# Performance work log

Measured on AMD Instinct MI355X. Metric: run time of the kernel, lower is better.

Reference implementation:

```python
import jax, jax.numpy as jnp
import numpy as np


def gcn_conv(x, W, b, src, dst, n_nodes):
    """PyG GCNConv: linear transform, add self-loops, symmetric deg^-1/2 norm, scatter-add, bias."""
    h = x @ W  # [N, out] transform first (out_dim <= in_dim keeps gather traffic low)
    loop = jnp.arange(n_nodes)
    s = jnp.concatenate([src, loop])  # sources incl. self-loops
    d = jnp.concatenate([dst, loop])  # targets incl. self-loops
    deg = jnp.zeros((n_nodes,), h.dtype).at[d].add(jnp.ones((), h.dtype))
    dinv = jax.lax.rsqrt(deg)  # deg >= 1 because of self-loops
    coef = (dinv[s] * dinv[d])[:, None]  # [E+N, 1]
    out = jax.ops.segment_sum(h[s] * coef, d, num_segments=n_nodes)
    return out + b


def setup_inputs() -> dict:
    key = jax.random.key(0)
    k1, k2, k3, k4 = jax.random.split(key, 4)
    N, E = 100000, 1600000
    IN, HID, OUT = 128, 64, 32
    x = jax.random.normal(k1, (N, IN), dtype=jnp.float32)
    edge_index = jax.random.randint(k2, (2, E), 0, N, dtype=jnp.int64)
    W1 = jax.random.normal(k3, (IN, HID), dtype=jnp.float32) * (1.0 / np.sqrt(IN))
    b1 = jnp.zeros((HID,), jnp.float32)
    W2 = jax.random.normal(k4, (HID, OUT), dtype=jnp.float32) * (1.0 / np.sqrt(HID))
    b2 = jnp.zeros((OUT,), jnp.float32)
    return {"x": x, "edge_index": edge_index, "W1": W1, "b1": b1, "W2": W2, "b2": b2}


def reference(x, edge_index, W1, b1, W2, b2):
    src, dst = edge_index[0], edge_index[1]
    n = x.shape[0]
    h = jax.nn.relu(gcn_conv(x, W1, b1, src, dst, n))
    return gcn_conv(h, W2, b2, src, dst, n)
```

## Files before the change

kernel.cpp:

```cpp
#include <hip/hip_runtime.h>
#include <hip/hip_bf16.h>


#define IN_DIM 128
#define HID_DIM 64
#define OUT_DIM 32
#define BSHIFT 8
#define BSIZE 256
#define BMASK 255
#define PEB 4096
#define CAPSHIFT 13

typedef __attribute__((ext_vector_type(2))) float v2f;

__device__ inline unsigned pack_bf16x2(float a, float b) {
    unsigned ua = __float_as_uint(a), ub = __float_as_uint(b);
    unsigned ra = (ua + 0x7fffu + ((ua >> 16) & 1u)) >> 16;
    unsigned rb = (ub + 0x7fffu + ((ub >> 16) & 1u)) & 0xffff0000u;
    return (ra & 0xffffu) | rb;
}
#define BF_LO(w) __uint_as_float((w) << 16)
#define BF_HI(w) __uint_as_float((w) & 0xffff0000u)

__device__ inline v2f bfpair(unsigned u) {
    v2f r;
    r.x = __uint_as_float(u << 16);
    r.y = __uint_as_float(u & 0xffff0000u);
    return r;
}

#define ACC8(q)                                         \
    do {                                                \
        acc[0] += BF_LO((q).x); acc[1] += BF_HI((q).x); \
        acc[2] += BF_LO((q).y); acc[3] += BF_HI((q).y); \
        acc[4] += BF_LO((q).z); acc[5] += BF_HI((q).z); \
        acc[6] += BF_LO((q).w); acc[7] += BF_HI((q).w); \
    } while (0)

__global__ __launch_bounds__(256) void k_partition(const int* __restrict__ src,
                                                   const int* __restrict__ dst, int E,
                                                   int* __restrict__ bfill,
                                                   unsigned* __restrict__ packed, int B) {
    __shared__ int cnt[512];
    __shared__ int off[512];
    int t = threadIdx.x;
    for (int b = t; b < 512; b += 256) cnt[b] = 0;
    __syncthreads();
    int base = blockIdx.x * PEB;
    int dv[PEB / 256];
#pragma unroll
    for (int i = 0; i < PEB / 256; ++i) {
        int e = base + i * 256 + t;
        dv[i] = (e < E) ? dst[e] : -1;
        if (dv[i] >= 0) atomicAdd(&cnt[dv[i] >> BSHIFT], 1);
    }
    __syncthreads();
    for (int b = t; b < B; b += 256) {
        int c = cnt[b];
        int o = c ? atomicAdd(&bfill[b], c) : 0;
        off[b] = (b << CAPSHIFT) + o;
    }
    __syncthreads();
#pragma unroll
    for (int i = 0; i < PEB / 256; ++i) {
        int e = base + i * 256 + t;
        int d = dv[i];
        if (d >= 0) {
            int s = src[e];
            int slot = atomicAdd(&off[d >> BSHIFT], 1);
            packed[slot] = ((unsigned)s << BSHIFT) | (unsigned)(d & BMASK);
        }
    }
}

__global__ __launch_bounds__(256) void k_csrfill(const unsigned* __restrict__ packed,
                                                 const int* __restrict__ bfill,
                                                 int* __restrict__ colidx,
                                                 uint2* __restrict__ rowptr2,
                                                 float* __restrict__ dinv,
                                                 int N, int B) {
    __shared__ int ldeg[256];
    __shared__ int lscan[256];
    __shared__ int sexc[256];
    __shared__ int lfill[256];
    int t = threadIdx.x, bkt = blockIdx.x;
    int base = bkt << CAPSHIFT;
    int end  = base + bfill[bkt];
    ldeg[t] = 0;
    __syncthreads();
    for (int e = base + t; e < end; e += 256)
        atomicAdd(&ldeg[packed[e] & BMASK], 1);
    __syncthreads();
    int v = ldeg[t];
    lscan[t] = v;
    __syncthreads();
    for (int off = 1; off < 256; off <<= 1) {
        int x = (t >= off) ? lscan[t - off] : 0;
        __syncthreads();
        lscan[t] += x;
        __syncthreads();
    }
    int exc = lscan[t] - v;
    sexc[t] = exc;
    lfill[t] = 0;
    int node = (bkt << BSHIFT) + t;
    if (node < N) {
        rowptr2[node] = make_uint2((unsigned)(base + exc), (unsigned)(base + exc + v));
        dinv[node] = rsqrtf((float)v + 1.0f);
    }
    __syncthreads();
    for (int e = base + t; e < end; e += 256) {
        unsigned w = packed[e];
        int ld = w & BMASK;
        int pos = base + sexc[ld] + atomicAdd(&lfill[ld], 1);
        colidx[pos] = (int)(w >> BSHIFT);
    }
}

__global__ __launch_bounds__(256) void k_gemm1(const float* __restrict__ x,
                                               const float* __restrict__ W,
                                               const float* __restrict__ dinv,
                                               unsigned* __restrict__ g1b, int N) {
    __shared__ float xs[64 * 36];
    __shared__ float ws[32 * 64];
    int t = threadIdx.x;
    int row0 = blockIdx.x * 64;
    int tx = t & 15;
    int ty = t >> 4;
    int sr = t >> 3, sc = t & 7;

    float acc[4][4] = {};
    for (int kt = 0; kt < 4; ++kt) {
        const float4* W4 = (const float4*)(W + kt * 32 * HID_DIM);
        float4* ws4 = (float4*)ws;
        ws4[t] = W4[t];
        ws4[t + 256] = W4[t + 256];
#pragma unroll
        for (int half = 0; half < 2; ++half) {
            int r = sr + half * 32;
            int row = row0 + r;
            float4 val = make_float4(0.f, 0.f, 0.f, 0.f);
            if (row < N)
                val = *(const float4*)&x[(size_t)row * IN_DIM + kt * 32 + sc * 4];
            *(float4*)&xs[r * 36 + sc * 4] = val;
        }
        __syncthreads();
#pragma unroll
        for (int k = 0; k < 32; k += 4) {
            float a[4][4], b[4][4];
#pragma unroll
            for (int i = 0; i < 4; ++i)
                *(float4*)a[i] = *(const float4*)&xs[(ty * 4 + i) * 36 + k];
#pragma unroll
            for (int kk = 0; kk < 4; ++kk)
                *(float4*)b[kk] = *(const float4*)&ws[(k + kk) * HID_DIM + tx * 4];
#pragma unroll
            for (int i = 0; i < 4; ++i)
#pragma unroll
                for (int kk = 0; kk < 4; ++kk)
#pragma unroll
                    for (int j = 0; j < 4; ++j)
                        acc[i][j] += a[i][kk] * b[kk][j];
        }
        __syncthreads();
    }
#pragma unroll
    for (int i = 0; i < 4; ++i) {
        int row = row0 + ty * 4 + i;
        if (row < N) {
            float dv = dinv[row];
            uint2 u;
            u.x = pack_bf16x2(acc[i][0] * dv, acc[i][1] * dv);
            u.y = pack_bf16x2(acc[i][2] * dv, acc[i][3] * dv);
            *(uint2*)&g1b[(size_t)row * 32 + tx * 2] = u;
        }
    }
}

__global__ __launch_bounds__(128) void k_agg1(const unsigned* __restrict__ g1,
                                              const uint2* __restrict__ rowptr2,
                                              const int* __restrict__ colidx,
                                              const float* __restrict__ dinv,
                                              const float* __restrict__ b1,
                                              unsigned* __restrict__ t1b, int N) {
    int t = threadIdx.x;
    int lane = t & 63;
    int q = lane >> 4, ql = lane & 15;
    int grp = ql >> 3, fp = ql & 7;
    int dd = blockIdx.x * 8 + (t >> 6) * 4 + q;
    bool live = dd < N;
    int d = live ? dd : N - 1;

    uint2 be = rowptr2[d];
    v2f a01 = {0.f, 0.f}, a23 = {0.f, 0.f}, a45 = {0.f, 0.f}, a67 = {0.f, 0.f};
#define ACC8V(qv)                                    \
    do {                                             \
        a01 += bfpair((qv).x); a23 += bfpair((qv).y);\
        a45 += bfpair((qv).z); a67 += bfpair((qv).w);\
    } while (0)
    int e = (int)be.x, end = (int)be.y;
    for (; e + 4 <= end; e += 4) {
        int s0 = colidx[e + grp];
        int s1 = colidx[e + 2 + grp];
        uint4 q0 = *(const uint4*)&g1[(size_t)s0 * 32 + fp * 4];
        uint4 q1 = *(const uint4*)&g1[(size_t)s1 * 32 + fp * 4];
        ACC8V(q0);
        ACC8V(q1);
    }
    for (; e + 2 <= end; e += 2) {
        int s = colidx[e + grp];
        uint4 qv = *(const uint4*)&g1[(size_t)s * 32 + fp * 4];
        ACC8V(qv);
    }
    if (e < end) {
        int s = colidx[e];
        uint4 qv = *(const uint4*)&g1[(size_t)s * 32 + fp * 4];
        if (grp == 0) ACC8V(qv);
    }
#undef ACC8V
    float acc[8] = {a01.x, a01.y, a23.x, a23.y, a45.x, a45.y, a67.x, a67.y};
#pragma unroll
    for (int i = 0; i < 8; ++i)
        acc[i] += __shfl_xor(acc[i], 8);

    uint4 sq = *(const uint4*)&g1[(size_t)d * 32 + fp * 4];
    ACC8(sq);
    float dv = dinv[d];
    float4 bb0 = ((const float4*)b1)[fp * 2];
    float4 bb1 = ((const float4*)b1)[fp * 2 + 1];
    float v0 = fmaxf(dv * acc[0] + bb0.x, 0.f);
    float v1 = fmaxf(dv * acc[1] + bb0.y, 0.f);
    float v2 = fmaxf(dv * acc[2] + bb0.z, 0.f);
    float v3 = fmaxf(dv * acc[3] + bb0.w, 0.f);
    float v4 = fmaxf(dv * acc[4] + bb1.x, 0.f);
    float v5 = fmaxf(dv * acc[5] + bb1.y, 0.f);
    float v6 = fmaxf(dv * acc[6] + bb1.z, 0.f);
    float v7 = fmaxf(dv * acc[7] + bb1.w, 0.f);
    if (live && grp == 0) {
        uint4 u;
        u.x = pack_bf16x2(v0, v1);
        u.y = pack_bf16x2(v2, v3);
        u.z = pack_bf16x2(v4, v5);
        u.w = pack_bf16x2(v6, v7);
        *(uint4*)&t1b[(size_t)dd * 32 + fp * 4] = u;
    }
}

__global__ __launch_bounds__(256) void k_gemm2b(const unsigned* __restrict__ t1b,
                                                const float* __restrict__ W2,
                                                const float* __restrict__ dinv,
                                                unsigned* __restrict__ g2b, int N) {
    __shared__ float t1s[64 * 68];
    __shared__ float W2s[HID_DIM * OUT_DIM];
    int t = threadIdx.x;
    int row0 = blockIdx.x * 64;

    const float4* W24 = (const float4*)W2;
    float4* W2s4 = (float4*)W2s;
    W2s4[t] = W24[t];
    W2s4[t + 256] = W24[t + 256];
#pragma unroll
    for (int i = 0; i < 8; ++i) {
        int idx = t + 256 * i;
        int r = idx >> 5, c = idx & 31;
        int grow = row0 + r;
        unsigned u = 0;
        if (grow < N) u = t1b[(size_t)grow * 32 + c];
        float2 f;
        f.x = BF_LO(u);
        f.y = BF_HI(u);
        *(float2*)&t1s[r * 68 + c * 2] = f;
    }
    __syncthreads();

    int ty = t >> 3;
    int tx = t & 7;
    float acc[2][4] = {};
#pragma unroll 4
    for (int k = 0; k < 64; k += 4) {
        float a[2][4], b[4][4];
#pragma unroll
        for (int i = 0; i < 2; ++i)
            *(float4*)a[i] = *(const float4*)&t1s[(ty * 2 + i) * 68 + k];
#pragma unroll
        for (int kk = 0; kk < 4; ++kk)
            *(float4*)b[kk] = *(const float4*)&W2s[(k + kk) * OUT_DIM + tx * 4];
#pragma unroll
        for (int i = 0; i < 2; ++i)
#pragma unroll
            for (int kk = 0; kk < 4; ++kk)
#pragma unroll
                for (int j = 0; j < 4; ++j)
                    acc[i][j] += a[i][kk] * b[kk][j];
    }
#pragma unroll
    for (int i = 0; i < 2; ++i) {
        int row = row0 + ty * 2 + i;
        if (row < N) {
            float dv = dinv[row];
            uint2 u;
            u.x = pack_bf16x2(acc[i][0] * dv, acc[i][1] * dv);
            u.y = pack_bf16x2(acc[i][2] * dv, acc[i][3] * dv);
            *(uint2*)&g2b[(size_t)row * 16 + tx * 2] = u;
        }
    }
}

__global__ __launch_bounds__(128) void k_agg2(const unsigned* __restrict__ g2,
                                              const uint2* __restrict__ rowptr2,
                                              const int* __restrict__ colidx,
                                              const float* __restrict__ dinv,
                                              const float* __restrict__ b2,
                                              float* __restrict__ out, int N) {
    int t = threadIdx.x;
    int lane = t & 63;
    int o = lane >> 3, ol = lane & 7;
    int grp = ol >> 2, fp = ol & 3;
    int dd = blockIdx.x * 16 + (t >> 6) * 8 + o;
    bool live = dd < N;
    int d = live ? dd : N - 1;

    uint2 be = rowptr2[d];
    v2f a01 = {0.f, 0.f}, a23 = {0.f, 0.f}, a45 = {0.f, 0.f}, a67 = {0.f, 0.f};
#define ACC8V(qv)                                    \
    do {                                             \
        a01 += bfpair((qv).x); a23 += bfpair((qv).y);\
        a45 += bfpair((qv).z); a67 += bfpair((qv).w);\
    } while (0)
    int e = (int)be.x, end = (int)be.y;
    for (; e + 4 <= end; e += 4) {
        int s0 = colidx[e + grp];
        int s1 = colidx[e + 2 + grp];
        uint4 q0 = *(const uint4*)&g2[(size_t)s0 * 16 + fp * 4];
        uint4 q1 = *(const uint4*)&g2[(size_t)s1 * 16 + fp * 4];
        ACC8V(q0);
        ACC8V(q1);
    }
    for (; e + 2 <= end; e += 2) {
        int s = colidx[e + grp];
        uint4 qv = *(const uint4*)&g2[(size_t)s * 16 + fp * 4];
        ACC8V(qv);
    }
    if (e < end) {
        int s = colidx[e];
        uint4 qv = *(const uint4*)&g2[(size_t)s * 16 + fp * 4];
        if (grp == 0) ACC8V(qv);
    }
#undef ACC8V
    float acc[8] = {a01.x, a01.y, a23.x, a23.y, a45.x, a45.y, a67.x, a67.y};
#pragma unroll
    for (int i = 0; i < 8; ++i)
        acc[i] += __shfl_xor(acc[i], 4);
    uint4 sq = *(const uint4*)&g2[(size_t)d * 16 + fp * 4];
    ACC8(sq);
    float dv = dinv[d];
    float4 bb0 = ((const float4*)b2)[fp * 2];
    float4 bb1 = ((const float4*)b2)[fp * 2 + 1];
    if (live && grp == 0) {
        float4 r0, r1;
        r0.x = dv * acc[0] + bb0.x; r0.y = dv * acc[1] + bb0.y;
        r0.z = dv * acc[2] + bb0.z; r0.w = dv * acc[3] + bb0.w;
        r1.x = dv * acc[4] + bb1.x; r1.y = dv * acc[5] + bb1.y;
        r1.z = dv * acc[6] + bb1.z; r1.w = dv * acc[7] + bb1.w;
        *(float4*)&out[(size_t)dd * OUT_DIM + fp * 8] = r0;
        *(float4*)&out[(size_t)dd * OUT_DIM + fp * 8 + 4] = r1;
    }
}

extern "C" void kernel_launch(void* const* d_in, const int* in_sizes, int n_in,
                              void* d_out, int out_size, void* d_ws, size_t ws_size,
                              hipStream_t stream) {
    const float* x  = (const float*)d_in[0];
    const int*   ei = (const int*)d_in[1];
    const float* W1 = (const float*)d_in[2];
    const float* b1 = (const float*)d_in[3];
    const float* W2 = (const float*)d_in[4];
    const float* b2 = (const float*)d_in[5];
    float* out = (float*)d_out;

    const int N = in_sizes[0] / IN_DIM;
    const int E = in_sizes[1] / 2;
    const int* src = ei;
    const int* dst = ei + E;

    const int B   = (N + BSIZE - 1) / BSIZE;
    const int nPB = (E + PEB - 1) / PEB;
    const size_t SLOTS = (size_t)B << CAPSHIFT;

    char* p = (char*)d_ws;
    auto alloc = [&](size_t bytes) -> void* {
        void* r = (void*)p;
        p += (bytes + 255) & ~(size_t)255;
        return r;
    };
    int*      bfill   = (int*)alloc((size_t)B * 4);
    unsigned* packed  = (unsigned*)alloc(SLOTS * 4);
    int*      colidx  = (int*)alloc(SLOTS * 4);
    uint2*    rowptr2 = (uint2*)alloc((size_t)N * 8);
    float*    dinv    = (float*)alloc((size_t)N * 4);
    unsigned* g1b     = (unsigned*)alloc((size_t)N * 32 * 4);
    unsigned* t1b     = (unsigned*)alloc((size_t)N * 32 * 4);
    unsigned* g2b     = (unsigned*)alloc((size_t)N * 16 * 4);

    hipMemsetAsync(bfill, 0, (size_t)B * 4, stream);
    k_partition<<<nPB, 256, 0, stream>>>(src, dst, E, bfill, packed, B);
    k_csrfill<<<B, 256, 0, stream>>>(packed, bfill, colidx, rowptr2, dinv, N, B);

    k_gemm1<<<(N + 63) / 64, 256, 0, stream>>>(x, W1, dinv, g1b, N);
    k_agg1<<<(N + 7) / 8, 128, 0, stream>>>(g1b, rowptr2, colidx, dinv, b1, t1b, N);
    k_gemm2b<<<(N + 63) / 64, 256, 0, stream>>>(t1b, W2, dinv, g2b, N);
    k_agg2<<<(N + 15) / 16, 128, 0, stream>>>(g2b, rowptr2, colidx, dinv, b2, out, N);
}
```

Baseline: 234.0 us.

## Rewrite first GEMM with bf16 MFMA 16x16x32 instructions

New measurement: 226.2 us. -3.3%, faster.

```diff
diff --git a/kernel.cpp b/kernel.cpp
--- a/kernel.cpp
+++ b/kernel.cpp
@@ -12,12 +12,18 @@
 #define CAPSHIFT 13
 
 typedef __attribute__((ext_vector_type(2))) float v2f;
+typedef __attribute__((ext_vector_type(8))) short short8v;
+typedef __attribute__((ext_vector_type(4))) float float4v;
 
 __device__ inline unsigned pack_bf16x2(float a, float b) {
     unsigned ua = __float_as_uint(a), ub = __float_as_uint(b);
     unsigned ra = (ua + 0x7fffu + ((ua >> 16) & 1u)) >> 16;
     unsigned rb = (ub + 0x7fffu + ((ub >> 16) & 1u)) & 0xffff0000u;
     return (ra & 0xffffu) | rb;
+}
+__device__ inline unsigned short f2bf(float f) {
+    unsigned u = __float_as_uint(f);
+    return (unsigned short)((u + 0x7fffu + ((u >> 16) & 1u)) >> 16);
 }
 #define BF_LO(w) __uint_as_float((w) << 16)
 #define BF_HI(w) __uint_as_float((w) & 0xffff0000u)
@@ -121,58 +127,53 @@
                                                const float* __restrict__ W,
                                                const float* __restrict__ dinv,
                                                unsigned* __restrict__ g1b, int N) {
-    __shared__ float xs[64 * 36];
-    __shared__ float ws[32 * 64];
+    __shared__ unsigned xs[16 * 66];
     int t = threadIdx.x;
-    int row0 = blockIdx.x * 64;
-    int tx = t & 15;
-    int ty = t >> 4;
-    int sr = t >> 3, sc = t & 7;
-
-    float acc[4][4] = {};
+    int row0 = blockIdx.x * 16;
+    int w = t >> 6, lane = t & 63;
+    int quad = lane >> 4, m = lane & 15;
+    int ncol = w * 16 + m;
+
+    union { unsigned u[4]; short8v s; } bf[4];
+#pragma unroll
     for (int kt = 0; kt < 4; ++kt) {
-        const float4* W4 = (const float4*)(W + kt * 32 * HID_DIM);
-        float4* ws4 = (float4*)ws;
-        ws4[t] = W4[t];
-        ws4[t + 256] = W4[t + 256];
-#pragma unroll
-        for (int half = 0; half < 2; ++half) {
-            int r = sr + half * 32;
-            int row = row0 + r;
-            float4 val = make_float4(0.f, 0.f, 0.f, 0.f);
-            if (row < N)
-                val = *(const float4*)&x[(size_t)row * IN_DIM + kt * 32 + sc * 4];
-            *(float4*)&xs[r * 36 + sc * 4] = val;
+#pragma unroll
+        for (int jp = 0; jp < 4; ++jp) {
+            int k0 = kt * 32 + quad * 8 + jp * 2;
+            float f0 = W[(size_t)k0 * HID_DIM + ncol];
+            float f1 = W[(size_t)(k0 + 1) * HID_DIM + ncol];
+            bf[kt].u[jp] = pack_bf16x2(f0, f1);
         }
-        __syncthreads();
-#pragma unroll
-        for (int k = 0; k < 32; k += 4) {
-            float a[4][4], b[4][4];
-#pragma unroll
-            for (int i = 0; i < 4; ++i)
-                *(float4*)a[i] = *(const float4*)&xs[(ty * 4 + i) * 36 + k];
-#pragma unroll
-            for (int kk = 0; kk < 4; ++kk)
-                *(float4*)b[kk] = *(const float4*)&ws[(k + kk) * HID_DIM + tx * 4];
-#pragma unroll
-            for (int i = 0; i < 4; ++i)
-#pragma unroll
-                for (int kk = 0; kk < 4; ++kk)
-#pragma unroll
-                    for (int j = 0; j < 4; ++j)
-                        acc[i][j] += a[i][kk] * b[kk][j];
-        }
-        __syncthreads();
-    }
-#pragma unroll
-    for (int i = 0; i < 4; ++i) {
-        int row = row0 + ty * 4 + i;
-        if (row < N) {
-            float dv = dinv[row];
-            uint2 u;
-            u.x = pack_bf16x2(acc[i][0] * dv, acc[i][1] * dv);
-            u.y = pack_bf16x2(acc[i][2] * dv, acc[i][3] * dv);
-            *(uint2*)&g1b[(size_t)row * 32 + tx * 2] = u;
+    }
+
+#pragma unroll
+    for (int i = 0; i < 2; ++i) {
+        int idx = t + 256 * i;
+        int r = idx >> 5, c4 = idx & 31;
+        int grow = row0 + r;
+        float4 f = make_float4(0.f, 0.f, 0.f, 0.f);
+        if (grow < N) f = ((const float4*)x)[(size_t)grow * 32 + c4];
+        xs[r * 66 + c4 * 2]     = pack_bf16x2(f.x, f.y);
+        xs[r * 66 + c4 * 2 + 1] = pack_bf16x2(f.z, f.w);
+    }
+    __syncthreads();
+
+    float4v acc = {0.f, 0.f, 0.f, 0.f};
+#pragma unroll
+    for (int kt = 0; kt < 4; ++kt) {
+        union { unsigned u[4]; short8v s; } af;
+        const unsigned* ap = &xs[m * 66 + kt * 16 + quad * 4];
+        af.u[0] = ap[0]; af.u[1] = ap[1]; af.u[2] = ap[2]; af.u[3] = ap[3];
+        acc = __builtin_amdgcn_mfma_f32_16x16x32_bf16(af.s, bf[kt].s, acc, 0, 0, 0);
+    }
+
+    unsigned short* g1s = (unsigned short*)g1b;
+#pragma unroll
+    for (int reg = 0; reg < 4; ++reg) {
+        int r = row0 + quad * 4 + reg;
+        if (r < N) {
+            float dv = dinv[r];
+            g1s[(size_t)r * HID_DIM + ncol] = f2bf(acc[reg] * dv);
         }
     }
 }
@@ -406,7 +407,7 @@
     k_partition<<<nPB, 256, 0, stream>>>(src, dst, E, bfill, packed, B);
     k_csrfill<<<B, 256, 0, stream>>>(packed, bfill, colidx, rowptr2, dinv, N, B);
 
-    k_gemm1<<<(N + 63) / 64, 256, 0, stream>>>(x, W1, dinv, g1b, N);
+    k_gemm1<<<(N + 15) / 16, 256, 0, stream>>>(x, W1, dinv, g1b, N);
     k_agg1<<<(N + 7) / 8, 128, 0, stream>>>(g1b, rowptr2, colidx, dinv, b1, t1b, N);
     k_gemm2b<<<(N + 63) / 64, 256, 0, stream>>>(t1b, W2, dinv, g2b, N);
     k_agg2<<<(N + 15) / 16, 128, 0, stream>>>(g2b, rowptr2, colidx, dinv, b2, out, N);
```
